# Kernel tuning notes

Measured on AMD Instinct MI355X. Metric: run time of the kernel, lower is better.

The kernel has to match this reference:

```python
import jax, jax.numpy as jnp
import numpy as np

B, DIM, H, W, HEAD = 8, 512, 32, 32, 8
DH = DIM // HEAD
N = H * W


def setup_inputs() -> dict:
    key = jax.random.key(0)
    ks = jax.random.split(key, 9)
    s = 0.05  # keep conv-weight scale modest so softmax logits are sane
    return {
        "x": jax.random.normal(ks[0], (B, DIM, H, W), jnp.float32),
        "wq_w": jax.random.normal(ks[1], (DIM, DIM), jnp.float32) * s,
        "wq_b": jax.random.normal(ks[2], (DIM,), jnp.float32) * s,
        "wk_w": jax.random.normal(ks[3], (DIM, DIM), jnp.float32) * s,
        "wk_b": jax.random.normal(ks[4], (DIM,), jnp.float32) * s,
        "wv_w": jax.random.normal(ks[5], (DIM, DIM), jnp.float32) * s,
        "wv_b": jax.random.normal(ks[6], (DIM,), jnp.float32) * s,
        "r_h": jax.random.normal(ks[7], (1, HEAD, DH, 1, H), jnp.float32),
        "r_w": jax.random.normal(ks[8], (1, HEAD, DH, W, 1), jnp.float32),
    }


def reference(x, wq_w, wq_b, wk_w, wk_b, wv_w, wv_b, r_h, r_w):
    b, dim, h, w = x.shape
    head = r_h.shape[1]
    dh = dim // head
    n = h * w

    def conv1x1(inp, wgt, bias):
        # 1x1 conv == channel-mixing matmul
        return jnp.einsum('bchw,oc->bohw', inp, wgt) + bias[None, :, None, None]

    q = conv1x1(x, wq_w, wq_b).reshape(b, head, dh, n).transpose(0, 1, 3, 2)  # [b,h,n,d]
    k = conv1x1(x, wk_w, wk_b).reshape(b, head, dh, n)                        # [b,h,d,n]
    v = conv1x1(x, wv_w, wv_b).reshape(b, head, dh, n)                        # [b,h,d,n]

    # relative position term: (1,head,dh,1,H)+(1,head,dh,W,1) -> (1,head,dh,W*H)
    r = (r_h + r_w).reshape(head, dh, n)

    content_position = jnp.einsum('bhnd,hdm->bhnm', q, r)
    content_content = jnp.einsum('bhnd,bhdm->bhnm', q, k)
    # faithful odd reduction: softmax over the whole flattened (head*n*n) per batch row
    energy = (content_content + content_position).reshape(b, -1)
    attention = jax.nn.softmax(energy, axis=-1).reshape(b, head, n, n)

    feature = jnp.einsum('bhdn,bhnm->bhdm', v, attention).reshape(b, dim, h, w)
    # AvgPool2d(kernel=2, stride=2)
    out = feature.reshape(b, dim, h // 2, 2, w // 2, 2).mean(axis=(3, 5))
    return out
```

## Files before the change

### kernel.cpp

```cpp
#include <hip/hip_runtime.h>
#include <hip/hip_bf16.h>
#include <math.h>

#define BB   8
#define DIMC 512
#define HEAD 8
#define DH   64
#define NN   1024
#define HW   32

typedef __attribute__((ext_vector_type(8))) __bf16 bf16x8;
typedef __attribute__((ext_vector_type(4))) float  f32x4;
typedef __attribute__((ext_vector_type(4))) short  short4v;

#define MFMA16(a, b, c) __builtin_amdgcn_mfma_f32_16x16x32_bf16((a), (b), (c), 0, 0, 0)

__device__ __forceinline__ f32x4 mfma_pv(short4v a, short4v b, f32x4 c) {
#if __has_builtin(__builtin_amdgcn_mfma_f32_16x16x16bf16_1k)
    return __builtin_amdgcn_mfma_f32_16x16x16bf16_1k(a, b, c, 0, 0, 0);
#else
    asm volatile("v_mfma_f32_16x16x16_bf16 %0, %1, %2, %0"
                 : "+v"(c) : "v"(a), "v"(b));
    return c;
#endif
}

__device__ __forceinline__ int SW(int row, int col) {
    return (row << 6) + (col ^ ((row & 7) << 3));
}

__device__ __forceinline__ unsigned short bfh(float v) {
    unsigned int u = __float_as_uint(v);
    return (unsigned short)((u + 0x7fffu + ((u >> 16) & 1u)) >> 16);
}
__device__ __forceinline__ float bf2f(unsigned short h) {
    return __uint_as_float(((unsigned int)h) << 16);
}

__global__ __launch_bounds__(256)
void prep_x(const float* __restrict__ x,
            unsigned short* __restrict__ XTh, unsigned short* __restrict__ XTl)
{
    const int tid = threadIdx.x;
    const int nt = blockIdx.x;
    const int ct = blockIdx.y;
    const int b  = blockIdx.z;
    const int c0 = ct << 6, n0 = nt << 6;

    __shared__ float XsT[64][68];

    #pragma unroll
    for (int p = 0; p < 4; ++p) {
        int idx = tid + (p << 8);
        int cr = idx >> 4;
        int nc4 = (idx & 15) << 2;
        float4 v = *(const float4*)&x[((size_t)b * DIMC + c0 + cr) * NN + n0 + nc4];
        XsT[nc4 + 0][cr] = v.x;
        XsT[nc4 + 1][cr] = v.y;
        XsT[nc4 + 2][cr] = v.z;
        XsT[nc4 + 3][cr] = v.w;
    }
    __syncthreads();
    #pragma unroll
    for (int p = 0; p < 4; ++p) {
        int idx = tid + (p << 8);
        int n = idx >> 4;
        int c4 = (idx & 15) << 2;
        float4 v = *(const float4*)&XsT[n][c4];
        float vv[4] = {v.x, v.y, v.z, v.w};
        union { unsigned short u[4]; uint2 w; } ph, pl;
        #pragma unroll
        for (int j = 0; j < 4; ++j) {
            unsigned short hh = bfh(vv[j]);
            ph.u[j] = hh;
            pl.u[j] = bfh(vv[j] - bf2f(hh));
        }
        size_t off = ((size_t)(b * NN + n0 + n)) * DIMC + c0 + c4;
        *(uint2*)&XTh[off] = ph.w;
        *(uint2*)&XTl[off] = pl.w;
    }
}

__global__ __launch_bounds__(256)
void prep_w(const float* __restrict__ wq, const float* __restrict__ wk,
            const float* __restrict__ wv,
            unsigned short* __restrict__ Wh, unsigned short* __restrict__ Wl)
{
    const int z = blockIdx.y;
    const float* src = (z == 0) ? wq : (z == 1) ? wk : wv;
    const size_t zb = (size_t)z * DIMC * DIMC;
    #pragma unroll
    for (int p = 0; p < 4; ++p) {
        size_t i = (size_t)blockIdx.x * 4096 + (p << 10) + (threadIdx.x << 2);
        float4 v = *(const float4*)&src[i];
        float vv[4] = {v.x, v.y, v.z, v.w};
        union { unsigned short u[4]; uint2 w; } ph, pl;
        #pragma unroll
        for (int j = 0; j < 4; ++j) {
            unsigned short hh = bfh(vv[j]);
            ph.u[j] = hh;
            pl.u[j] = bfh(vv[j] - bf2f(hh));
        }
        *(uint2*)&Wh[zb + i] = ph.w;
        *(uint2*)&Wl[zb + i] = pl.w;
    }
}

__global__ __launch_bounds__(256)
void qkv_gemm(const unsigned short* __restrict__ XTh, const unsigned short* __restrict__ XTl,
              const unsigned short* __restrict__ Wh, const unsigned short* __restrict__ Wl,
              const float* __restrict__ wq_b, const float* __restrict__ wk_b,
              const float* __restrict__ wv_b,
              const float* __restrict__ r_h, const float* __restrict__ r_w,
              unsigned short* __restrict__ Qh, unsigned short* __restrict__ Ql,
              unsigned short* __restrict__ Kh, unsigned short* __restrict__ Kl,
              unsigned short* __restrict__ Vh, unsigned short* __restrict__ Vl)
{
    const int tid = threadIdx.x;
    const int z = blockIdx.z, hd = blockIdx.y;
    const int gn = blockIdx.x << 7;
    const int b = gn >> 10, posb = gn & 1023;
    const int oB = hd << 6;
    const int lane = tid & 63, w = tid >> 6;

    __shared__ __align__(16) unsigned short sm[24576];
    unsigned short* Ah = sm;
    unsigned short* Al = sm + 4096;
    unsigned short* Bh = sm + 8192;
    unsigned short* Bl = sm + 16384;

    const float* bias = (z == 0) ? wq_b : (z == 1) ? wk_b : wv_b;
    const unsigned short* wsh = Wh + (size_t)z * DIMC * DIMC + (size_t)oB * DIMC;
    const unsigned short* wsl = Wl + (size_t)z * DIMC * DIMC + (size_t)oB * DIMC;
    const unsigned short* xth = XTh + ((size_t)(b * NN + posb)) * DIMC;
    const unsigned short* xtl = XTl + ((size_t)(b * NN + posb)) * DIMC;

    f32x4 acc[8];
    #pragma unroll
    for (int t = 0; t < 8; ++t) acc[t] = (f32x4){0.f, 0.f, 0.f, 0.f};

    for (int ks = 0; ks < 8; ++ks) {
        const int c0 = ks << 6;
        #pragma unroll
        for (int p = 0; p < 2; ++p) {
            int idx = (p << 8) + tid;
            int row = idx >> 3, col8 = (idx & 7) << 3;
            size_t g = (size_t)row * DIMC + c0 + col8;
            *(float4*)&Ah[SW(row, col8)] = *(const float4*)&wsh[g];
            *(float4*)&Al[SW(row, col8)] = *(const float4*)&wsl[g];
        }
        #pragma unroll
        for (int p = 0; p < 4; ++p) {
            int idx = (p << 8) + tid;
            int row = idx >> 3, col8 = (idx & 7) << 3;
            size_t g = (size_t)row * DIMC + c0 + col8;
            *(float4*)&Bh[SW(row, col8)] = *(const float4*)&xth[g];
            *(float4*)&Bl[SW(row, col8)] = *(const float4*)&xtl[g];
        }
        __syncthreads();

        const int ar = (w << 4) + (lane & 15);
        const int kc = (lane >> 4) << 3;
        bf16x8 ah[2], al[2];
        ah[0] = *(const bf16x8*)&Ah[SW(ar, kc)];
        ah[1] = *(const bf16x8*)&Ah[SW(ar, 32 + kc)];
        al[0] = *(const bf16x8*)&Al[SW(ar, kc)];
        al[1] = *(const bf16x8*)&Al[SW(ar, 32 + kc)];
        #pragma unroll
        for (int t = 0; t < 8; ++t) {
            int br = (t << 4) + (lane & 15);
            #pragma unroll
            for (int s = 0; s < 2; ++s) {
                bf16x8 xh = *(const bf16x8*)&Bh[SW(br, s * 32 + kc)];
                bf16x8 xl = *(const bf16x8*)&Bl[SW(br, s * 32 + kc)];
                acc[t] = MFMA16(ah[s], xh, acc[t]);
                acc[t] = MFMA16(ah[s], xl, acc[t]);
                acc[t] = MFMA16(al[s], xh, acc[t]);
            }
        }
        __syncthreads();
    }

    float* F = (float*)sm;
    #pragma unroll
    for (int t = 0; t < 8; ++t) {
        int n = (t << 4) + (lane & 15);
        #pragma unroll
        for (int r = 0; r < 4; ++r) {
            int o = (w << 4) + ((lane >> 4) << 2) + r;
            F[o * 132 + n] = acc[t][r];
        }
    }
    __syncthreads();

    const size_t bh = (size_t)(b * HEAD + hd);
    if (z != 2) {
        unsigned short* Dh = (z == 0) ? Qh : Kh;
        unsigned short* Dl = (z == 0) ? Ql : Kl;
        #pragma unroll
        for (int p = 0; p < 8; ++p) {
            int idx = (p << 8) + tid;
            int n = idx >> 4, d0 = (idx & 15) << 2;
            union { unsigned short u[4]; uint2 v; } ph, pl;
            #pragma unroll
            for (int i = 0; i < 4; ++i) {
                int d = d0 + i;
                float val = F[d * 132 + n] + bias[oB + d];
                if (z == 1) {
                    int m = posb + n;
                    val += r_h[(size_t)(oB + d) * HW + (m & 31)]
                         + r_w[(size_t)(oB + d) * HW + (m >> 5)];
                }
                unsigned short hh = bfh(val);
                ph.u[i] = hh;
                pl.u[i] = bfh(val - bf2f(hh));
            }
            size_t off = (((size_t)bh * NN + posb + n) << 6) + d0;
            *(uint2*)&Dh[off] = ph.v;
            *(uint2*)&Dl[off] = pl.v;
        }
    } else {
        #pragma unroll
        for (int p = 0; p < 8; ++p) {
            int idx = (p << 8) + tid;
            int d = idx >> 5, n0 = (idx & 31) << 2;
            float4 v = *(const float4*)&F[d * 132 + n0];
            float vv[4] = {v.x, v.y, v.z, v.w};
            float bia = bias[oB + d];
            union { unsigned short u[4]; uint2 w2; } ph, pl;
            #pragma unroll
            for (int j = 0; j < 4; ++j) {
                float val = vv[j] + bia;
                unsigned short hh = bfh(val);
                ph.u[j] = hh;
                pl.u[j] = bfh(val - bf2f(hh));
            }
            size_t off = (((size_t)bh << 6) + d) * NN + posb + n0;
            *(uint2*)&Vh[off] = ph.w2;
            *(uint2*)&Vl[off] = pl.w2;
        }
    }
}

__global__ __launch_bounds__(256, 2)
void flash_pv(const unsigned short* __restrict__ Qh, const unsigned short* __restrict__ Ql,
              const unsigned short* __restrict__ Kh, const unsigned short* __restrict__ Kl,
              const unsigned short* __restrict__ Vh, const unsigned short* __restrict__ Vl,
              float* __restrict__ pooled, float* __restrict__ pstats)
{
    const int tid = threadIdx.x;
    const int mt = blockIdx.x, hd = blockIdx.y, b = blockIdx.z;
    const int bh = b * HEAD + hd;
    const int lane = tid & 63, w = tid >> 6;
    const int r0 = lane & 15, c0 = (lane >> 4) << 3;

    __shared__ __align__(16) unsigned char smraw[2 * 64 * 65 * 4];
    unsigned short* Vsh = (unsigned short*)smraw;
    unsigned short* Vsl = Vsh + 4096;
    float* F0 = (float*)smraw;
    float* F1 = F0 + 64 * 65;
    __shared__ float bm[4], bs[4];

    const unsigned short* kh = Kh + (((size_t)bh * NN + (mt << 6)) << 6);
    const unsigned short* kl = Kl + (((size_t)bh * NN + (mt << 6)) << 6);
    bf16x8 kfh[4][2], kfl[4][2];
    #pragma unroll
    for (int t = 0; t < 4; ++t)
        #pragma unroll
        for (int s = 0; s < 2; ++s) {
            int off = (((t << 4) + r0) << 6) + (s << 5) + c0;
            kfh[t][s] = *(const bf16x8*)&kh[off];
            kfl[t][s] = *(const bf16x8*)&kl[off];
        }

    const unsigned short* qh = Qh + (((size_t)bh * NN) << 6);
    const unsigned short* ql = Ql + (((size_t)bh * NN) << 6);
    const unsigned short* vh = Vh + (((size_t)bh << 6) * NN);
    const unsigned short* vl = Vl + (((size_t)bh << 6) * NN);

    float m_w = -1e30f;
    float s_r = 0.f;

    f32x4 facc[4][4];
    #pragma unroll
    for (int u = 0; u < 4; ++u)
        #pragma unroll
        for (int t = 0; t < 4; ++t) facc[u][t] = (f32x4){0.f, 0.f, 0.f, 0.f};

    for (int nt = 0; nt < 16; ++nt) {
        const int nB = nt << 6;
        #pragma unroll
        for (int p = 0; p < 2; ++p) {
            int idx = (p << 8) + tid;
            int row = idx >> 3, c8 = (idx & 7) << 3;
            *(float4*)&Vsh[SW(row, c8)] = *(const float4*)&vh[(size_t)row * NN + nB + c8];
            *(float4*)&Vsl[SW(row, c8)] = *(const float4*)&vl[(size_t)row * NN + nB + c8];
        }
        const int qrow = nB + (w << 4) + r0;
        const size_t qb = ((size_t)qrow << 6) + c0;
        bf16x8 ah0 = *(const bf16x8*)&qh[qb];
        bf16x8 ah1 = *(const bf16x8*)&qh[qb + 32];
        bf16x8 al0 = *(const bf16x8*)&ql[qb];
        bf16x8 al1 = *(const bf16x8*)&ql[qb + 32];
        __syncthreads();

        f32x4 sacc[4];
        #pragma unroll
        for (int t = 0; t < 4; ++t) sacc[t] = (f32x4){0.f, 0.f, 0.f, 0.f};
        #pragma unroll
        for (int t = 0; t < 4; ++t) {
            sacc[t] = MFMA16(ah0, kfh[t][0], sacc[t]);
            sacc[t] = MFMA16(ah0, kfl[t][0], sacc[t]);
            sacc[t] = MFMA16(al0, kfh[t][0], sacc[t]);
        }
        #pragma unroll
        for (int t = 0; t < 4; ++t) {
            sacc[t] = MFMA16(ah1, kfh[t][1], sacc[t]);
            sacc[t] = MFMA16(ah1, kfl[t][1], sacc[t]);
            sacc[t] = MFMA16(al1, kfh[t][1], sacc[t]);
        }

        float tmax = -1e30f;
        #pragma unroll
        for (int t = 0; t < 4; ++t)
            #pragma unroll
            for (int r = 0; r < 4; ++r) tmax = fmaxf(tmax, sacc[t][r]);
        #pragma unroll
        for (int off = 1; off < 64; off <<= 1)
            tmax = fmaxf(tmax, __shfl_xor(tmax, off, 64));
        if (tmax > m_w) {
            float sc = __expf(m_w - tmax);
            s_r *= sc;
            #pragma unroll
            for (int u = 0; u < 4; ++u)
                #pragma unroll
                for (int t = 0; t < 4; ++t) facc[u][t] *= sc;
            m_w = tmax;
        }

        short4v pah[4], pal[4];
        #pragma unroll
        for (int t = 0; t < 4; ++t) {
            union { unsigned short u[4]; short4v v; } Ph, Pl;
            #pragma unroll
            for (int r = 0; r < 4; ++r) {
                float a = __expf(sacc[t][r] - m_w);
                s_r += a;
                unsigned short hh = bfh(a);
                Ph.u[r] = hh;
                Pl.u[r] = bfh(a - bf2f(hh));
            }
            pah[t] = Ph.v;
            pal[t] = Pl.v;
        }

        const int vcol = (w << 4) + ((lane >> 4) << 2);
        #pragma unroll
        for (int u = 0; u < 4; ++u) {
            int vrow = (u << 4) + r0;
            short4v vah = *(const short4v*)&Vsh[SW(vrow, vcol)];
            short4v vbl = *(const short4v*)&Vsl[SW(vrow, vcol)];
            #pragma unroll
            for (int t = 0; t < 4; ++t) {
                facc[u][t] = mfma_pv(vah, pah[t], facc[u][t]);
                facc[u][t] = mfma_pv(vbl, pah[t], facc[u][t]);
                facc[u][t] = mfma_pv(vah, pal[t], facc[u][t]);
            }
        }
        __syncthreads();
    }

    #pragma unroll
    for (int off = 1; off < 64; off <<= 1) s_r += __shfl_xor(s_r, off, 64);
    if (lane == 0) { bm[w] = m_w; bs[w] = s_r; }
    __syncthreads();
    const float m_B = fmaxf(fmaxf(bm[0], bm[1]), fmaxf(bm[2], bm[3]));
    const float s_B = bs[0] * __expf(bm[0] - m_B) + bs[1] * __expf(bm[1] - m_B)
                    + bs[2] * __expf(bm[2] - m_B) + bs[3] * __expf(bm[3] - m_B);
    const float fsc = __expf(m_w - m_B);
    #pragma unroll
    for (int u = 0; u < 4; ++u)
        #pragma unroll
        for (int t = 0; t < 4; ++t) facc[u][t] *= fsc;
    if (tid == 0) {
        pstats[((b << 7) + (hd << 4) + mt) * 2 + 0] = m_B;
        pstats[((b << 7) + (hd << 4) + mt) * 2 + 1] = s_B;
    }

    const int fr = (lane >> 4) << 2;
    if (w < 2) {
        float* Fw = (w == 0) ? F0 : F1;
        #pragma unroll
        for (int u = 0; u < 4; ++u)
            #pragma unroll
            for (int t = 0; t < 4; ++t)
                #pragma unroll
                for (int r = 0; r < 4; ++r)
                    Fw[((u << 4) + fr + r) * 65 + (t << 4) + r0] = facc[u][t][r];
    }
    __syncthreads();
    if (w >= 2) {
        float* Fw = (w == 2) ? F0 : F1;
        #pragma unroll
        for (int u = 0; u < 4; ++u)
            #pragma unroll
            for (int t = 0; t < 4; ++t)
                #pragma unroll
                for (int r = 0; r < 4; ++r)
                    Fw[((u << 4) + fr + r) * 65 + (t << 4) + r0] += facc[u][t][r];
    }
    __syncthreads();
    #pragma unroll
    for (int q = 0; q < 4; ++q) {
        int idx = (tid << 2) + q;
        int d = idx >> 4, wo = idx & 15;
        int m0 = wo << 1;
        float v = 0.25f * ((F0[d * 65 + m0]      + F1[d * 65 + m0]) +
                           (F0[d * 65 + m0 + 1]  + F1[d * 65 + m0 + 1]) +
                           (F0[d * 65 + 32 + m0] + F1[d * 65 + 32 + m0]) +
                           (F0[d * 65 + 33 + m0] + F1[d * 65 + 33 + m0]));
        pooled[(((size_t)(b * DIMC + (hd << 6) + d) << 4) + mt) * 16 + wo] = v;
    }
}

__global__ __launch_bounds__(128)
void combine_kernel(const float* __restrict__ pstats, float* __restrict__ gstats)
{
    const int b = blockIdx.x, tid = threadIdx.x;
    __shared__ float rm[128], rs[128];
    rm[tid] = pstats[((b << 7) + tid) * 2 + 0];
    rs[tid] = pstats[((b << 7) + tid) * 2 + 1];
    __syncthreads();
    for (int off = 64; off > 0; off >>= 1) {
        if (tid < off) {
            float m2 = rm[tid + off], s2 = rs[tid + off];
            float M = fmaxf(rm[tid], m2);
            rs[tid] = rs[tid] * __expf(rm[tid] - M) + s2 * __expf(m2 - M);
            rm[tid] = M;
        }
        __syncthreads();
    }
    if (tid == 0) { gstats[b * 2] = rm[0]; gstats[b * 2 + 1] = rs[0]; }
}

__global__ __launch_bounds__(256)
void finalize(const float* __restrict__ pooled, const float* __restrict__ pstats,
              const float* __restrict__ gstats, float* __restrict__ out)
{
    const int j = blockIdx.x * 256 + threadIdx.x;
    const int e = j << 2;
    const int mt = (e >> 4) & 15;
    const int c  = e >> 8;
    const int b  = c >> 9;
    const int hd = (c >> 6) & 7;
    const int sidx = (b << 7) + (hd << 4) + mt;
    const float s = __expf(pstats[sidx * 2] - gstats[b * 2]) / gstats[b * 2 + 1];
    float4 v = *(const float4*)&pooled[e];
    v.x *= s; v.y *= s; v.z *= s; v.w *= s;
    *(float4*)&out[e] = v;
}

extern "C" void kernel_launch(void* const* d_in, const int* in_sizes, int n_in,
                              void* d_out, int out_size, void* d_ws, size_t ws_size,
                              hipStream_t stream)
{
    const float* x    = (const float*)d_in[0];
    const float* wq_w = (const float*)d_in[1];
    const float* wq_b = (const float*)d_in[2];
    const float* wk_w = (const float*)d_in[3];
    const float* wk_b = (const float*)d_in[4];
    const float* wv_w = (const float*)d_in[5];
    const float* wv_b = (const float*)d_in[6];
    const float* r_h  = (const float*)d_in[7];
    const float* r_w  = (const float*)d_in[8];
    float* out = (float*)d_out;

    const size_t PRN = (size_t)BB * HEAD * NN * DH;
    const size_t WSZ = (size_t)3 * DIMC * DIMC;
    unsigned short* Qh  = (unsigned short*)d_ws;
    unsigned short* Ql  = Qh + PRN;
    unsigned short* Kh  = Ql + PRN;
    unsigned short* Kl  = Kh + PRN;
    unsigned short* Vh  = Kl + PRN;
    unsigned short* Vl  = Vh + PRN;
    unsigned short* XTh = Vl + PRN;
    unsigned short* XTl = XTh + PRN;
    unsigned short* Wh  = XTl + PRN;
    unsigned short* Wl  = Wh + WSZ;
    float* pstats = (float*)(Wl + WSZ);
    float* gstats = pstats + BB * 128 * 2;
    float* pooled = (float*)XTh;

    prep_x<<<dim3(16, 8, 8), 256, 0, stream>>>(x, XTh, XTl);
    prep_w<<<dim3(64, 3), 256, 0, stream>>>(wq_w, wk_w, wv_w, Wh, Wl);
    qkv_gemm<<<dim3(64, 8, 3), 256, 0, stream>>>(XTh, XTl, Wh, Wl,
                                                 wq_b, wk_b, wv_b, r_h, r_w,
                                                 Qh, Ql, Kh, Kl, Vh, Vl);
    flash_pv<<<dim3(16, 8, 8), 256, 0, stream>>>(Qh, Ql, Kh, Kl, Vh, Vl,
                                                 pooled, pstats);
    combine_kernel<<<dim3(8), 128, 0, stream>>>(pstats, gstats);
    finalize<<<dim3(1024), 256, 0, stream>>>(pooled, pstats, gstats, out);
}
```

Measured before the change: 250.3 us.

## Double-buffer V tiles in shared memory and raise occupancy bound

Splits shared memory into two V buffers so the next V tile is loaded while the current one feeds the QK/PV MFMAs, removing one barrier per tile from the critical path. The loop is unrolled by two around a factored tile_step helper. Launch bounds move from 2 to 4 blocks per CU, which caps registers per thread and may cause spills given the large K-fragment and accumulator register footprint.

```diff
diff --git a/kernel.cpp b/kernel.cpp
--- a/kernel.cpp
+++ b/kernel.cpp
@@ -242,7 +242,100 @@
     }
 }
 
-__global__ __launch_bounds__(256, 2)
+#define STAGE_V(nB, Dh, Dl)                                                        \
+    {                                                                              \
+        _Pragma("unroll")                                                          \
+        for (int p = 0; p < 2; ++p) {                                              \
+            int idx = (p << 8) + tid;                                              \
+            int row = idx >> 3, c8 = (idx & 7) << 3;                               \
+            *(float4*)&(Dh)[SW(row, c8)] =                                         \
+                *(const float4*)&vh[(size_t)row * NN + (nB) + c8];                 \
+            *(float4*)&(Dl)[SW(row, c8)] =                                         \
+                *(const float4*)&vl[(size_t)row * NN + (nB) + c8];                 \
+        }                                                                          \
+    }
+
+__device__ __forceinline__ void tile_step(
+    int nB, int w, int r0, int c0, int tid,
+    const unsigned short* __restrict__ qh, const unsigned short* __restrict__ ql,
+    const bf16x8 (&kfh)[4][2], const bf16x8 (&kfl)[4][2],
+    const unsigned short* Vsh, const unsigned short* Vsl,
+    float& m_w, float& s_r, f32x4 (&facc)[4][4])
+{
+    const int qrow = nB + (w << 4) + r0;
+    const size_t qb = ((size_t)qrow << 6) + c0;
+    bf16x8 ah0 = *(const bf16x8*)&qh[qb];
+    bf16x8 ah1 = *(const bf16x8*)&qh[qb + 32];
+    bf16x8 al0 = *(const bf16x8*)&ql[qb];
+    bf16x8 al1 = *(const bf16x8*)&ql[qb + 32];
+
+    f32x4 sacc[4];
+    #pragma unroll
+    for (int t = 0; t < 4; ++t) sacc[t] = (f32x4){0.f, 0.f, 0.f, 0.f};
+    #pragma unroll
+    for (int t = 0; t < 4; ++t) {
+        sacc[t] = MFMA16(ah0, kfh[t][0], sacc[t]);
+        sacc[t] = MFMA16(ah0, kfl[t][0], sacc[t]);
+        sacc[t] = MFMA16(al0, kfh[t][0], sacc[t]);
+    }
+    #pragma unroll
+    for (int t = 0; t < 4; ++t) {
+        sacc[t] = MFMA16(ah1, kfh[t][1], sacc[t]);
+        sacc[t] = MFMA16(ah1, kfl[t][1], sacc[t]);
+        sacc[t] = MFMA16(al1, kfh[t][1], sacc[t]);
+    }
+
+    float tmax = -1e30f;
+    #pragma unroll
+    for (int t = 0; t < 4; ++t)
+        #pragma unroll
+        for (int r = 0; r < 4; ++r) tmax = fmaxf(tmax, sacc[t][r]);
+    #pragma unroll
+    for (int off = 1; off < 64; off <<= 1)
+        tmax = fmaxf(tmax, __shfl_xor(tmax, off, 64));
+    if (tmax > m_w) {
+        float sc = __expf(m_w - tmax);
+        s_r *= sc;
+        #pragma unroll
+        for (int u = 0; u < 4; ++u)
+            #pragma unroll
+            for (int t = 0; t < 4; ++t) facc[u][t] *= sc;
+        m_w = tmax;
+    }
+
+    short4v pah[4], pal[4];
+    #pragma unroll
+    for (int t = 0; t < 4; ++t) {
+        union { unsigned short u[4]; short4v v; } Ph, Pl;
+        #pragma unroll
+        for (int r = 0; r < 4; ++r) {
+            float a = __expf(sacc[t][r] - m_w);
+            s_r += a;
+            unsigned short hh = bfh(a);
+            Ph.u[r] = hh;
+            Pl.u[r] = bfh(a - bf2f(hh));
+        }
+        pah[t] = Ph.v;
+        pal[t] = Pl.v;
+    }
+
+    const int lane_hi = (tid & 63) >> 4;
+    const int vcol = (w << 4) + (lane_hi << 2);
+    #pragma unroll
+    for (int u = 0; u < 4; ++u) {
+        int vrow = (u << 4) + r0;
+        short4v vah = *(const short4v*)&Vsh[SW(vrow, vcol)];
+        short4v vbl = *(const short4v*)&Vsl[SW(vrow, vcol)];
+        #pragma unroll
+        for (int t = 0; t < 4; ++t) {
+            facc[u][t] = mfma_pv(vah, pah[t], facc[u][t]);
+            facc[u][t] = mfma_pv(vbl, pah[t], facc[u][t]);
+            facc[u][t] = mfma_pv(vah, pal[t], facc[u][t]);
+        }
+    }
+}
+
+__global__ __launch_bounds__(256, 4)
 void flash_pv(const unsigned short* __restrict__ Qh, const unsigned short* __restrict__ Ql,
               const unsigned short* __restrict__ Kh, const unsigned short* __restrict__ Kl,
               const unsigned short* __restrict__ Vh, const unsigned short* __restrict__ Vl,
@@ -255,8 +348,10 @@
     const int r0 = lane & 15, c0 = (lane >> 4) << 3;
 
     __shared__ __align__(16) unsigned char smraw[2 * 64 * 65 * 4];
-    unsigned short* Vsh = (unsigned short*)smraw;
-    unsigned short* Vsl = Vsh + 4096;
+    unsigned short* VshA = (unsigned short*)smraw;
+    unsigned short* VslA = VshA + 4096;
+    unsigned short* VshB = VshA + 8192;
+    unsigned short* VslB = VshA + 12288;
     float* F0 = (float*)smraw;
     float* F1 = F0 + 64 * 65;
     __shared__ float bm[4], bs[4];
@@ -287,86 +382,18 @@
         #pragma unroll
         for (int t = 0; t < 4; ++t) facc[u][t] = (f32x4){0.f, 0.f, 0.f, 0.f};
 
-    for (int nt = 0; nt < 16; ++nt) {
-        const int nB = nt << 6;
-        #pragma unroll
-        for (int p = 0; p < 2; ++p) {
-            int idx = (p << 8) + tid;
-            int row = idx >> 3, c8 = (idx & 7) << 3;
-            *(float4*)&Vsh[SW(row, c8)] = *(const float4*)&vh[(size_t)row * NN + nB + c8];
-            *(float4*)&Vsl[SW(row, c8)] = *(const float4*)&vl[(size_t)row * NN + nB + c8];
-        }
-        const int qrow = nB + (w << 4) + r0;
-        const size_t qb = ((size_t)qrow << 6) + c0;
-        bf16x8 ah0 = *(const bf16x8*)&qh[qb];
-        bf16x8 ah1 = *(const bf16x8*)&qh[qb + 32];
-        bf16x8 al0 = *(const bf16x8*)&ql[qb];
-        bf16x8 al1 = *(const bf16x8*)&ql[qb + 32];
+    STAGE_V(0, VshA, VslA);
+    __syncthreads();
+
+    for (int ntp = 0; ntp < 8; ++ntp) {
+        const int nt0 = ntp << 1;
+        STAGE_V((nt0 + 1) << 6, VshB, VslB);
+        tile_step(nt0 << 6, w, r0, c0, tid, qh, ql, kfh, kfl, VshA, VslA,
+                  m_w, s_r, facc);
         __syncthreads();
-
-        f32x4 sacc[4];
-        #pragma unroll
-        for (int t = 0; t < 4; ++t) sacc[t] = (f32x4){0.f, 0.f, 0.f, 0.f};
-        #pragma unroll
-        for (int t = 0; t < 4; ++t) {
-            sacc[t] = MFMA16(ah0, kfh[t][0], sacc[t]);
-            sacc[t] = MFMA16(ah0, kfl[t][0], sacc[t]);
-            sacc[t] = MFMA16(al0, kfh[t][0], sacc[t]);
-        }
-        #pragma unroll
-        for (int t = 0; t < 4; ++t) {
-            sacc[t] = MFMA16(ah1, kfh[t][1], sacc[t]);
-            sacc[t] = MFMA16(ah1, kfl[t][1], sacc[t]);
-            sacc[t] = MFMA16(al1, kfh[t][1], sacc[t]);
-        }
-
-        float tmax = -1e30f;
-        #pragma unroll
-        for (int t = 0; t < 4; ++t)
-            #pragma unroll
-            for (int r = 0; r < 4; ++r) tmax = fmaxf(tmax, sacc[t][r]);
-        #pragma unroll
-        for (int off = 1; off < 64; off <<= 1)
-            tmax = fmaxf(tmax, __shfl_xor(tmax, off, 64));
-        if (tmax > m_w) {
-            float sc = __expf(m_w - tmax);
-            s_r *= sc;
-            #pragma unroll
-            for (int u = 0; u < 4; ++u)
-                #pragma unroll
-                for (int t = 0; t < 4; ++t) facc[u][t] *= sc;
-            m_w = tmax;
-        }
-
-        short4v pah[4], pal[4];
-        #pragma unroll
-        for (int t = 0; t < 4; ++t) {
-            union { unsigned short u[4]; short4v v; } Ph, Pl;
-            #pragma unroll
-            for (int r = 0; r < 4; ++r) {
-                float a = __expf(sacc[t][r] - m_w);
-                s_r += a;
-                unsigned short hh = bfh(a);
-                Ph.u[r] = hh;
-                Pl.u[r] = bfh(a - bf2f(hh));
-            }
-            pah[t] = Ph.v;
-            pal[t] = Pl.v;
-        }
-
-        const int vcol = (w << 4) + ((lane >> 4) << 2);
-        #pragma unroll
-        for (int u = 0; u < 4; ++u) {
-            int vrow = (u << 4) + r0;
-            short4v vah = *(const short4v*)&Vsh[SW(vrow, vcol)];
-            short4v vbl = *(const short4v*)&Vsl[SW(vrow, vcol)];
-            #pragma unroll
-            for (int t = 0; t < 4; ++t) {
-                facc[u][t] = mfma_pv(vah, pah[t], facc[u][t]);
-                facc[u][t] = mfma_pv(vbl, pah[t], facc[u][t]);
-                facc[u][t] = mfma_pv(vah, pal[t], facc[u][t]);
-            }
-        }
+        if (ntp < 7) STAGE_V((nt0 + 2) << 6, VshA, VslA);
+        tile_step((nt0 + 1) << 6, w, r0, c0, tid, qh, ql, kfh, kfl, VshB, VslB,
+                  m_w, s_r, facc);
         __syncthreads();
     }
 
```

Result: slower. 422.9 us (+68.9%).
